# Performance work log

Measured on AMD Instinct MI355X. Metric: run time of the kernel, lower is better.

## Reference

```python
import jax, jax.numpy as jnp
import numpy as np

KH = KW = 5          # deformable kernel (matches offset_channels = 2*5*5)
PAD = 2              # (5-1)//2
DG = 4               # deformable groups


def conv3d(x, w, padding, bias=None):
    # x: [N,C,D,H,W], w: [O,I,kd,kh,kw]
    out = jax.lax.conv_general_dilated(
        x, w, window_strides=(1, 1, 1), padding=padding,
        dimension_numbers=('NCDHW', 'OIDHW', 'NCDHW'))
    if bias is not None:
        out = out + bias[None, :, None, None, None]
    return out


def deform_conv2d(x, offset, weight, pad=PAD, dg=DG):
    """torchvision/mmcv-style deformable conv, stride 1, groups=1, no bias.
    x: [N,C,H,W]; offset: [N, dg*2*K, H, W] ordered (group, k, (dy,dx));
    weight: [Cout, C, KH, KW]."""
    N, C, H, W = x.shape
    K = KH * KW
    off = offset.reshape(N, dg, K, 2, H, W)
    ky, kx = jnp.meshgrid(jnp.arange(KH), jnp.arange(KW), indexing='ij')
    ky = ky.reshape(K).astype(x.dtype)
    kx = kx.reshape(K).astype(x.dtype)
    # absolute sampling positions: [N,dg,K,H,W]
    base_y = ky[:, None, None] - pad + jnp.arange(H, dtype=x.dtype)[None, :, None]
    base_x = kx[:, None, None] - pad + jnp.arange(W, dtype=x.dtype)[None, None, :]
    sy = base_y[None, None] + off[:, :, :, 0]
    sx = base_x[None, None] + off[:, :, :, 1]
    y0 = jnp.floor(sy)
    x0 = jnp.floor(sx)
    wy = sy - y0
    wx = sx - x0
    y0i = y0.astype(jnp.int32)
    x0i = x0.astype(jnp.int32)
    Cg = C // dg
    xg = x.reshape(N, dg, Cg, H * W)

    def gather(yi, xi):
        valid = (yi >= 0) & (yi < H) & (xi >= 0) & (xi < W)
        yc = jnp.clip(yi, 0, H - 1)
        xc = jnp.clip(xi, 0, W - 1)
        idx = (yc * W + xc).reshape(N, dg, 1, K * H * W)
        v = jnp.take_along_axis(xg, idx, axis=3).reshape(N, dg, Cg, K, H, W)
        return v * valid[:, :, None].astype(x.dtype)

    v00 = gather(y0i, x0i)
    v01 = gather(y0i, x0i + 1)
    v10 = gather(y0i + 1, x0i)
    v11 = gather(y0i + 1, x0i + 1)
    wy_ = wy[:, :, None]
    wx_ = wx[:, :, None]
    samp = (v00 * (1 - wy_) * (1 - wx_) + v01 * (1 - wy_) * wx_
            + v10 * wy_ * (1 - wx_) + v11 * wy_ * wx_)
    samp = samp.reshape(N, C, K, H, W)             # deform groups only affect offsets
    wmat = weight.reshape(weight.shape[0], C, K)
    return jnp.einsum('nckhw,ock->nohw', samp, wmat)


def setup_inputs() -> dict:
    key = jax.random.key(0)
    k0, k1, k2, k3, k4 = jax.random.split(key, 5)
    bs, C, T, H, W = 1, 256, 4, 48, 48
    x = jax.random.normal(k0, (bs, C, T, H, W), dtype=jnp.float32)
    # spatio_offset: Conv3d(C -> dg*2*K, kernel (1,5,5), pad (0,2,2), no bias)
    w_off = jax.random.normal(k1, (DG * 2 * KH * KW, C, 1, KH, KW), dtype=jnp.float32) * 0.01
    # spatio_adaption: DeformConv2d weight, init std=0.01 (per init_weights)
    w_def = jax.random.normal(k2, (C, C, KH, KW), dtype=jnp.float32) * 0.01
    # temporal: Conv3d(C -> C, kernel (3,3,3), pad (1,1,1), with bias)
    fan_in = C * 27
    w_temp = jax.random.normal(k3, (C, C, 3, 3, 3), dtype=jnp.float32) * (1.0 / np.sqrt(fan_in))
    b_temp = jax.random.normal(k4, (C,), dtype=jnp.float32) * 0.01
    return {'x': x, 'w_off': w_off, 'w_def': w_def, 'w_temp': w_temp, 'b_temp': b_temp}


def reference(x, w_off, w_def, w_temp, b_temp):
    bs, C, T, H, W = x.shape
    # offset branch uses detached input (torch: x.detach())
    offset = conv3d(jax.lax.stop_gradient(x), w_off, [(0, 0), (PAD, PAD), (PAD, PAD)])
    off_fold = offset.transpose(0, 2, 1, 3, 4).reshape(bs * T, -1, H, W)
    x_fold = x.transpose(0, 2, 1, 3, 4).reshape(bs * T, C, H, W)
    x_spatio_fold = deform_conv2d(x_fold, off_fold, w_def)
    x_spatio = x_spatio_fold.reshape(bs, T, C, H, W).transpose(0, 2, 1, 3, 4)
    # cascaded=False branch: temporal conv on original x, then residual sum
    x_temporal = conv3d(x, w_temp, [(1, 1), (1, 1), (1, 1)], b_temp)
    return x_spatio + x_temporal
```

## Files before the change

### kernel.cpp

```cpp
#include <hip/hip_runtime.h>
#include <hip/hip_bf16.h>

#define T    4
#define C    256
#define H    48
#define W    48
#define HW   2304
#define OFFC 200
#define CK5  6400
#define CK9  2304
#define NFULL 9216
#define BPAD 72

typedef __attribute__((ext_vector_type(8))) short bf16x8;
typedef __attribute__((ext_vector_type(4))) float f32x4;

__device__ __forceinline__ unsigned short f2bf(float f) {
    unsigned int u = __float_as_uint(f);
    return (unsigned short)((u + 0x7FFFu + ((u >> 16) & 1u)) >> 16);
}
__device__ __forceinline__ float bflo(unsigned int v) { return __uint_as_float(v << 16); }
__device__ __forceinline__ float bfhi(unsigned int v) { return __uint_as_float(v & 0xFFFF0000u); }
__device__ __forceinline__ unsigned int pack2(float lo, float hi) {
    __hip_bfloat162 h = __float22bfloat162_rn(make_float2(lo, hi));
    return *reinterpret_cast<unsigned int*>(&h);
}
__device__ __forceinline__ void gload16(const void* g, void* l) {
    __builtin_amdgcn_global_load_lds(
        (const __attribute__((address_space(1))) unsigned int*)g,
        (__attribute__((address_space(3))) unsigned int*)l, 16, 0, 0);
}

__global__ __launch_bounds__(256) void prep_xt_k(const float* __restrict__ x,
                                                 const float* __restrict__ w_off,
                                                 const float* __restrict__ w_def,
                                                 const float* __restrict__ w_temp,
                                                 const float* __restrict__ bias,
                                                 unsigned short* __restrict__ wbo,
                                                 unsigned short* __restrict__ wbd,
                                                 unsigned short* __restrict__ wbT,
                                                 float* __restrict__ offb,
                                                 float* __restrict__ out,
                                                 unsigned short* __restrict__ xt) {
    __shared__ float tile[64][65];
    if (blockIdx.x >= 24320) {
        const int zb = blockIdx.x - 24320;
        const int p0 = (zb % 36) * 64, c0 = ((zb / 36) & 3) * 64, t = zb / 144;
        const int px = threadIdx.x & 63, sub = threadIdx.x >> 6;
        for (int cl = sub; cl < 64; cl += 4)
            tile[px][cl] = x[((long)(c0 + cl) * T + t) * HW + p0 + px];
        __syncthreads();
        const int seg = sub * 16;
        unsigned int pk[8];
        #pragma unroll
        for (int d = 0; d < 8; ++d)
            pk[d] = pack2(tile[px][seg + d * 2], tile[px][seg + d * 2 + 1]);
        unsigned short* orow = xt + ((long)t * HW + p0 + px) * 256 + c0 + seg;
        *(uint4*)(orow + 0) = make_uint4(pk[0], pk[1], pk[2], pk[3]);
        *(uint4*)(orow + 8) = make_uint4(pk[4], pk[5], pk[6], pk[7]);
        return;
    }
    long i = (long)blockIdx.x * 256 + threadIdx.x;
    if (i < 1638400) {
        const int c = (int)(i & 255); const int rest = (int)(i >> 8);
        const int q = rest % 25, o = rest / 25;
        wbo[(long)o * CK5 + q * 256 + c] =
            (o < OFFC) ? f2bf(w_off[((long)o * 256 + c) * 25 + q]) : (unsigned short)0;
    } else if (i < 3276800) {
        i -= 1638400;
        const int c = (int)(i & 255); const int rest = (int)(i >> 8);
        const int q = rest % 25, o = rest / 25;
        wbd[(long)o * CK5 + q * 256 + c] = f2bf(w_def[((long)o * 256 + c) * 25 + q]);
    } else if (i < 5046272) {
        i -= 3276800;
        const int c = (int)(i & 255); const int rest = (int)(i >> 8);
        const int j = rest % 9, oo = rest / 9;
        const int o = oo & 255, kt = oo >> 8;
        wbT[(long)kt * (256 * CK9) + (long)o * CK9 + j * 256 + c] =
            f2bf(w_temp[((long)o * 256 + c) * 27 + kt * 9 + j]);
    } else if (i < 5636096) {
        i -= 5046272;
        ((float4*)offb)[i] = make_float4(0.f, 0.f, 0.f, 0.f);
    } else {
        i -= 5636096;
        const float b = bias[(int)(i / 2304)];
        ((float4*)out)[i] = make_float4(b, b, b, b);
    }
}

__device__ __forceinline__ void mfma_iter_w(const unsigned short* __restrict__ Asl,
                                            const unsigned short* __restrict__ Bsl,
                                            int wave, int quad, int l16, f32x4 acc[4][4]) {
    const int wm = (wave & 1) * 64, wn = (wave >> 1) * 64;
    #pragma unroll
    for (int kh = 0; kh < 2; ++kh) {
        bf16x8 af[4], bfr[4];
        #pragma unroll
        for (int ii = 0; ii < 4; ++ii) {
            const int row = wm + ii * 16 + l16;
            const int slot = (kh * 4 + quad + (l16 & 7)) & 7;
            af[ii] = *(const bf16x8*)(Asl + row * 64 + slot * 8);
        }
        #pragma unroll
        for (int j = 0; j < 4; ++j)
            bfr[j] = *(const bf16x8*)(Bsl + (wn + j * 16 + l16) * BPAD + kh * 32 + quad * 8);
        #pragma unroll
        for (int ii = 0; ii < 4; ++ii)
            #pragma unroll
            for (int j = 0; j < 4; ++j)
                acc[ii][j] = __builtin_amdgcn_mfma_f32_16x16x32_bf16(af[ii], bfr[j], acc[ii][j], 0, 0, 0);
    }
}
__device__ __forceinline__ void epilogue_atomic_w(float* __restrict__ Cf, int m0, int n0,
                                                  int wave, int quad, int l16,
                                                  int Mvalid, f32x4 acc[4][4]) {
    const int wm = (wave & 1) * 64, wn = (wave >> 1) * 64;
    #pragma unroll
    for (int i = 0; i < 4; ++i)
        #pragma unroll
        for (int rr = 0; rr < 4; ++rr) {
            const int o = m0 + wm + i * 16 + quad * 4 + rr;
            if (o >= Mvalid) continue;
            #pragma unroll
            for (int j = 0; j < 4; ++j)
                unsafeAtomicAdd(Cf + (long)o * NFULL + n0 + wn + j * 16 + l16, acc[i][j][rr]);
        }
}

__global__ __launch_bounds__(256, 4) void gemm_off_k(const unsigned short* __restrict__ A,
                                                     const unsigned short* __restrict__ xt,
                                                     float* __restrict__ Cf) {
    __shared__ unsigned short Asl[128 * 64];
    __shared__ unsigned short Bsl[128 * BPAD];
    const int tid = threadIdx.x;
    const int wave = tid >> 6, lane = tid & 63;
    const int quad = lane >> 4, l16 = lane & 15;
    const int n0 = blockIdx.x * 128, m0 = blockIdx.y * 128, k0 = blockIdx.z * 640;
    const int t = n0 / HW, p0 = n0 - t * HW;

    const int r8 = lane >> 3, s8 = lane & 7;
    const int qg = (s8 - r8) & 7;
    const long ldAb = (long)CK5 * 2;
    const char* Ap = (const char*)A + (long)(m0 + wave * 32 + r8) * ldAb
                     + (long)k0 * 2 + qg * 16;
    const long rstep8 = 8 * ldAb;
    unsigned short* la = Asl + wave * 2048;

    const int px = tid >> 1, half = tid & 1;
    const int p = p0 + px, h = p / 48, w = p - h * 48;
    const unsigned short* xts = xt + (long)t * HW * 256 + half * 32;

    auto produce = [&](int kk, uint4 v[4]) {
        const int q = kk >> 8, cb = kk & 255;
        const int d = q / 5;
        const int y = h + d - 2, xx = w + (q - d * 5) - 2;
        v[0] = make_uint4(0u, 0u, 0u, 0u); v[1] = v[0]; v[2] = v[0]; v[3] = v[0];
        if ((y >= 0) & (y < 48) & (xx >= 0) & (xx < 48)) {
            const unsigned short* bp = xts + (y * 48 + xx) * 256 + cb;
            #pragma unroll
            for (int d4 = 0; d4 < 4; ++d4) v[d4] = *(const uint4*)(bp + d4 * 8);
        }
    };

    uint4 cv[4];
    produce(k0, cv);

    f32x4 acc[4][4] = {};
    for (int i = 0; i < 10; ++i) {
        __syncthreads();
        #pragma unroll
        for (int c2 = 0; c2 < 4; ++c2) gload16(Ap + c2 * rstep8, la + c2 * 512);
        Ap += 128;
        #pragma unroll
        for (int d4 = 0; d4 < 4; ++d4)
            *(uint4*)(Bsl + px * BPAD + half * 32 + d4 * 8) = cv[d4];
        __syncthreads();
        if (i + 1 < 10) produce(k0 + (i + 1) * 64, cv);
        mfma_iter_w(Asl, Bsl, wave, quad, l16, acc);
    }
    epilogue_atomic_w(Cf, m0, n0, wave, quad, l16, OFFC, acc);
}

__device__ __forceinline__ void mfma_iter(const unsigned short* __restrict__ Asl,
                                          const unsigned short* __restrict__ Bsl,
                                          int wave, int quad, int l16, f32x4 acc[4][2]) {
    const int wm = (wave & 1) * 64, wn = (wave >> 1) * 32;
    #pragma unroll
    for (int kh = 0; kh < 2; ++kh) {
        bf16x8 af[4], bfr[2];
        #pragma unroll
        for (int i = 0; i < 4; ++i) {
            const int row = wm + i * 16 + l16;
            const int slot = (kh * 4 + quad + (l16 & 7)) & 7;
            af[i] = *(const bf16x8*)(Asl + row * 64 + slot * 8);
        }
        #pragma unroll
        for (int j = 0; j < 2; ++j)
            bfr[j] = *(const bf16x8*)(Bsl + (wn + j * 16 + l16) * BPAD + kh * 32 + quad * 8);
        #pragma unroll
        for (int i = 0; i < 4; ++i)
            #pragma unroll
            for (int j = 0; j < 2; ++j)
                acc[i][j] = __builtin_amdgcn_mfma_f32_16x16x32_bf16(af[i], bfr[j], acc[i][j], 0, 0, 0);
    }
}
__device__ __forceinline__ void epilogue_atomic(float* __restrict__ Cf, int m0, int n0,
                                                int wave, int quad, int l16,
                                                int Mvalid, f32x4 acc[4][2]) {
    const int wm = (wave & 1) * 64, wn = (wave >> 1) * 32;
    #pragma unroll
    for (int i = 0; i < 4; ++i)
        #pragma unroll
        for (int rr = 0; rr < 4; ++rr) {
            const int o = m0 + wm + i * 16 + quad * 4 + rr;
            if (o >= Mvalid) continue;
            #pragma unroll
            for (int j = 0; j < 2; ++j)
                unsafeAtomicAdd(Cf + (long)o * NFULL + n0 + wn + j * 16 + l16, acc[i][j][rr]);
        }
}

__device__ __forceinline__ void pos_calc(int h, int w, int q, float dy, float dx,
                                         float wgt[4], int idx[4]) {
    const int d = q / 5;
    const int qy = d - 2, qx = q - d * 5 - 2;
    const float sy = (float)(h + qy) + dy;
    const float sx = (float)(w + qx) + dx;
    const float y0f = floorf(sy), x0f = floorf(sx);
    const float wy = sy - y0f, wx = sx - x0f;
    const int y0 = (int)y0f, x0 = (int)x0f;
    const int y1 = y0 + 1, x1 = x0 + 1;
    float w00 = (1.f - wy) * (1.f - wx);
    float w01 = (1.f - wy) * wx;
    float w10 = wy * (1.f - wx);
    float w11 = wy * wx;
    const bool vy0 = (y0 >= 0) & (y0 < 48), vy1 = (y1 >= 0) & (y1 < 48);
    const bool vx0 = (x0 >= 0) & (x0 < 48), vx1 = (x1 >= 0) & (x1 < 48);
    if (!(vy0 & vx0)) w00 = 0.f;
    if (!(vy0 & vx1)) w01 = 0.f;
    if (!(vy1 & vx0)) w10 = 0.f;
    if (!(vy1 & vx1)) w11 = 0.f;
    const int yc0 = min(max(y0, 0), 47), yc1 = min(max(y1, 0), 47);
    const int xc0 = min(max(x0, 0), 47), xc1 = min(max(x1, 0), 47);
    wgt[0] = w00; wgt[1] = w01; wgt[2] = w10; wgt[3] = w11;
    idx[0] = yc0 * 48 + xc0; idx[1] = yc0 * 48 + xc1;
    idx[2] = yc1 * 48 + xc0; idx[3] = yc1 * 48 + xc1;
}
__device__ __forceinline__ uint4 blend4(const uint4 u[4], const float wgt[4]) {
    unsigned int pk[4];
    #pragma unroll
    for (int qi = 0; qi < 4; ++qi) {
        const unsigned int a = ((const unsigned int*)&u[0])[qi];
        const unsigned int b = ((const unsigned int*)&u[1])[qi];
        const unsigned int c = ((const unsigned int*)&u[2])[qi];
        const unsigned int d = ((const unsigned int*)&u[3])[qi];
        const float rl = wgt[0] * bflo(a) + wgt[1] * bflo(b) + wgt[2] * bflo(c) + wgt[3] * bflo(d);
        const float rh = wgt[0] * bfhi(a) + wgt[1] * bfhi(b) + wgt[2] * bfhi(c) + wgt[3] * bfhi(d);
        pk[qi] = pack2(rl, rh);
    }
    return make_uint4(pk[0], pk[1], pk[2], pk[3]);
}

__device__ __forceinline__ void gemm_def_body(unsigned short* __restrict__ Asl,
                                              unsigned short* __restrict__ Bsl,
                                              const unsigned short* __restrict__ A,
                                              const unsigned short* __restrict__ xt,
                                              const float* __restrict__ offb,
                                              float* __restrict__ Cf,
                                              int m0, int n0, int k0) {
    const int tid = threadIdx.x;
    const int wave = tid >> 6, lane = tid & 63;
    const int quad = lane >> 4, l16 = lane & 15;
    const int t = n0 / HW, p0 = n0 - t * HW;
    const int px = tid >> 2, seg = tid & 3;
    const int p = p0 + px, h = p / 48, w = p - h * 48;
    const int nabs = n0 + px;
    const unsigned short* xts = xt + (long)t * HW * 256 + seg * 8;

    const int r8 = lane >> 3, s8 = lane & 7;
    const int qg = (s8 - r8) & 7;
    const long ldAb = (long)CK5 * 2;
    const char* Ap = (const char*)A + (long)(m0 + wave * 32 + r8) * ldAb
                     + (long)k0 * 2 + qg * 16;
    const long rstep8 = 8 * ldAb;
    unsigned short* la = Asl + wave * 2048;

    auto off_load = [&](int kk, float& dy, float& dx) {
        const int q = kk >> 8, g = (kk & 255) >> 6;
        dy = offb[(long)(g * 50 + 2 * q) * NFULL + nabs];
        dx = offb[(long)(g * 50 + 2 * q + 1) * NFULL + nabs];
    };
    auto corners = [&](int kk, float dy, float dx, uint4 u[8], float wgt[4]) {
        const int cb = kk & 255;
        int idx[4];
        pos_calc(h, w, kk >> 8, dy, dx, wgt, idx);
        #pragma unroll
        for (int cn = 0; cn < 4; ++cn) {
            const unsigned short* bp = xts + idx[cn] * 256 + cb;
            u[cn]     = *(const uint4*)bp;
            u[cn + 4] = *(const uint4*)(bp + 32);
        }
    };

    uint4 pkv0, pkv1;
    float dyN, dxN;
    {
        float dy0, dx0;
        off_load(k0, dy0, dx0);
        uint4 u[8]; float wg[4];
        corners(k0, dy0, dx0, u, wg);
        pkv0 = blend4(u, wg);
        pkv1 = blend4(u + 4, wg);
        off_load(k0 + 64, dyN, dxN);
    }

    f32x4 acc[4][2] = {};
    for (int i = 0; i < 20; ++i) {
        const int kk = k0 + i * 64;
        __syncthreads();
        #pragma unroll
        for (int c2 = 0; c2 < 4; ++c2) gload16(Ap + c2 * rstep8, la + c2 * 512);
        Ap += 128;
        *(uint4*)(Bsl + px * BPAD + seg * 8)      = pkv0;
        *(uint4*)(Bsl + px * BPAD + 32 + seg * 8) = pkv1;
        __syncthreads();
        const bool more = (i + 1 < 20);
        uint4 u[8]; float wg[4];
        if (more) {
            corners(kk + 64, dyN, dxN, u, wg);
            if (i + 2 < 20) off_load(kk + 128, dyN, dxN);
        }
        mfma_iter(Asl, Bsl, wave, quad, l16, acc);
        if (more) {
            pkv0 = blend4(u, wg);
            pkv1 = blend4(u + 4, wg);
        }
    }
    epilogue_atomic(Cf, m0, n0, wave, quad, l16, C, acc);
}

__device__ __forceinline__ void gemm_temp_body(unsigned short* __restrict__ Asl,
                                               unsigned short* __restrict__ Bsl,
                                               const unsigned short* __restrict__ A,
                                               const unsigned short* __restrict__ xt, int tsrc,
                                               float* __restrict__ Cf,
                                               int m0, int n0, int k0) {
    const int tid = threadIdx.x;
    const int wave = tid >> 6, lane = tid & 63;
    const int quad = lane >> 4, l16 = lane & 15;
    const int t = n0 / HW, p0 = n0 - t * HW;
    const int px = tid >> 1, half = tid & 1;
    const int p = p0 + px, h = p / 48, w = p - h * 48;
    const unsigned short* xts = xt + (long)tsrc * HW * 256 + half * 32;

    const int r8 = lane >> 3, s8 = lane & 7;
    const int qg = (s8 - r8) & 7;
    const long ldAb = (long)CK9 * 2;
    const char* Ap = (const char*)A + (long)(m0 + wave * 32 + r8) * ldAb
                     + (long)k0 * 2 + qg * 16;
    const long rstep8 = 8 * ldAb;
    unsigned short* la = Asl + wave * 2048;

    auto produce = [&](int kk, uint4 v[4]) {
        const int q = kk >> 8, cb = kk & 255;
        const int d = q / 3;
        const int y = h + d - 1, xx = w + (q - d * 3) - 1;
        v[0] = make_uint4(0u, 0u, 0u, 0u); v[1] = v[0]; v[2] = v[0]; v[3] = v[0];
        if ((y >= 0) & (y < 48) & (xx >= 0) & (xx < 48)) {
            const unsigned short* bp = xts + (y * 48 + xx) * 256 + cb;
            #pragma unroll
            for (int d4 = 0; d4 < 4; ++d4) v[d4] = *(const uint4*)(bp + d4 * 8);
        }
    };

    uint4 cv[4];
    produce(k0, cv);

    f32x4 acc[4][4] = {};
    for (int i = 0; i < 18; ++i) {
        __syncthreads();
        #pragma unroll
        for (int c2 = 0; c2 < 4; ++c2) gload16(Ap + c2 * rstep8, la + c2 * 512);
        Ap += 128;
        #pragma unroll
        for (int d4 = 0; d4 < 4; ++d4)
            *(uint4*)(Bsl + px * BPAD + half * 32 + d4 * 8) = cv[d4];
        __syncthreads();
        if (i + 1 < 18) produce(k0 + (i + 1) * 64, cv);
        mfma_iter_w(Asl, Bsl, wave, quad, l16, acc);
    }
    epilogue_atomic_w(Cf, m0, n0, wave, quad, l16, C, acc);
}

__global__ __launch_bounds__(256, 4) void gemm_dt_k(const unsigned short* __restrict__ wbd,
                                                    const unsigned short* __restrict__ wbT,
                                                    const unsigned short* __restrict__ xt,
                                                    const float* __restrict__ offb,
                                                    float* __restrict__ out) {
    __shared__ unsigned short Asl[128 * 64];
    __shared__ unsigned short Bsl[128 * BPAD];
    const int z = blockIdx.z, m0 = blockIdx.y * 128;
    if (z < 5) {
        const int n0 = blockIdx.x * 64;
        gemm_def_body(Asl, Bsl, wbd, xt, offb, out, m0, n0, z * 1280);
    } else {
        if (blockIdx.x >= 72) return;
        const int n0 = blockIdx.x * 128;
        const int zz = z - 5, kt = zz >> 1, half = zz & 1;
        const int t = n0 / HW, tsrc = t + kt - 1;
        if (tsrc < 0 || tsrc >= T) return;
        gemm_temp_body(Asl, Bsl, wbT + (long)kt * 256 * CK9, xt, tsrc, out,
                       m0, n0, half * 1152);
    }
}

extern "C" void kernel_launch(void* const* d_in, const int* in_sizes, int n_in,
                              void* d_out, int out_size, void* d_ws, size_t ws_size,
                              hipStream_t stream) {
    const float* x      = (const float*)d_in[0];
    const float* w_off  = (const float*)d_in[1];
    const float* w_def  = (const float*)d_in[2];
    const float* w_temp = (const float*)d_in[3];
    const float* b_temp = (const float*)d_in[4];
    float* out = (float*)d_out;

    unsigned short* xt   = (unsigned short*)d_ws;
    float*          offb = (float*)((char*)d_ws + 4718592ul);
    unsigned short* wbo  = (unsigned short*)((char*)d_ws + 14155776ul);
    unsigned short* wbd  = (unsigned short*)((char*)d_ws + 17432576ul);
    unsigned short* wbT  = (unsigned short*)((char*)d_ws + 20709376ul);

    prep_xt_k<<<24896, 256, 0, stream>>>(x, w_off, w_def, w_temp, b_temp,
                                         wbo, wbd, wbT, offb, out, xt);
    gemm_off_k<<<dim3(72, 2, 10), 256, 0, stream>>>(wbo, xt, offb);
    gemm_dt_k<<<dim3(144, 2, 11), 256, 0, stream>>>(wbd, wbT, xt, offb, out);
}
```

Baseline: 318.0 us.

## Rebalance temporal-conv GEMM across launches and co-schedule with offset GEMM

The temporal conv taps kt=0 and kt=2 move into the offset-conv GEMM launch, which becomes one fused kernel with 14 z-slices. Only the centre tap kt=1 stays alongside the deformable GEMM, now on 64-wide N tiles with 4x2 accumulators instead of 128-wide. This spreads work more evenly between the two launches and keeps fewer idle or early-exiting blocks in the second grid. The cost is a larger first launch and more atomic traffic from the smaller tiles.

```diff
diff --git a/kernel.cpp b/kernel.cpp
--- a/kernel.cpp
+++ b/kernel.cpp
@@ -127,15 +127,54 @@
         }
 }
 
-__global__ __launch_bounds__(256, 4) void gemm_off_k(const unsigned short* __restrict__ A,
-                                                     const unsigned short* __restrict__ xt,
-                                                     float* __restrict__ Cf) {
-    __shared__ unsigned short Asl[128 * 64];
-    __shared__ unsigned short Bsl[128 * BPAD];
+__device__ __forceinline__ void mfma_iter(const unsigned short* __restrict__ Asl,
+                                          const unsigned short* __restrict__ Bsl,
+                                          int wave, int quad, int l16, f32x4 acc[4][2]) {
+    const int wm = (wave & 1) * 64, wn = (wave >> 1) * 32;
+    #pragma unroll
+    for (int kh = 0; kh < 2; ++kh) {
+        bf16x8 af[4], bfr[2];
+        #pragma unroll
+        for (int i = 0; i < 4; ++i) {
+            const int row = wm + i * 16 + l16;
+            const int slot = (kh * 4 + quad + (l16 & 7)) & 7;
+            af[i] = *(const bf16x8*)(Asl + row * 64 + slot * 8);
+        }
+        #pragma unroll
+        for (int j = 0; j < 2; ++j)
+            bfr[j] = *(const bf16x8*)(Bsl + (wn + j * 16 + l16) * BPAD + kh * 32 + quad * 8);
+        #pragma unroll
+        for (int i = 0; i < 4; ++i)
+            #pragma unroll
+            for (int j = 0; j < 2; ++j)
+                acc[i][j] = __builtin_amdgcn_mfma_f32_16x16x32_bf16(af[i], bfr[j], acc[i][j], 0, 0, 0);
+    }
+}
+__device__ __forceinline__ void epilogue_atomic(float* __restrict__ Cf, int m0, int n0,
+                                                int wave, int quad, int l16,
+                                                int Mvalid, f32x4 acc[4][2]) {
+    const int wm = (wave & 1) * 64, wn = (wave >> 1) * 32;
+    #pragma unroll
+    for (int i = 0; i < 4; ++i)
+        #pragma unroll
+        for (int rr = 0; rr < 4; ++rr) {
+            const int o = m0 + wm + i * 16 + quad * 4 + rr;
+            if (o >= Mvalid) continue;
+            #pragma unroll
+            for (int j = 0; j < 2; ++j)
+                unsafeAtomicAdd(Cf + (long)o * NFULL + n0 + wn + j * 16 + l16, acc[i][j][rr]);
+        }
+}
+
+__device__ __forceinline__ void gemm_off_body(unsigned short* __restrict__ Asl,
+                                              unsigned short* __restrict__ Bsl,
+                                              const unsigned short* __restrict__ A,
+                                              const unsigned short* __restrict__ xt,
+                                              float* __restrict__ Cf,
+                                              int m0, int n0, int k0) {
     const int tid = threadIdx.x;
     const int wave = tid >> 6, lane = tid & 63;
     const int quad = lane >> 4, l16 = lane & 15;
-    const int n0 = blockIdx.x * 128, m0 = blockIdx.y * 128, k0 = blockIdx.z * 640;
     const int t = n0 / HW, p0 = n0 - t * HW;
 
     const int r8 = lane >> 3, s8 = lane & 7;
@@ -181,43 +220,108 @@
     epilogue_atomic_w(Cf, m0, n0, wave, quad, l16, OFFC, acc);
 }
 
-__device__ __forceinline__ void mfma_iter(const unsigned short* __restrict__ Asl,
-                                          const unsigned short* __restrict__ Bsl,
-                                          int wave, int quad, int l16, f32x4 acc[4][2]) {
-    const int wm = (wave & 1) * 64, wn = (wave >> 1) * 32;
-    #pragma unroll
-    for (int kh = 0; kh < 2; ++kh) {
-        bf16x8 af[4], bfr[2];
-        #pragma unroll
-        for (int i = 0; i < 4; ++i) {
-            const int row = wm + i * 16 + l16;
-            const int slot = (kh * 4 + quad + (l16 & 7)) & 7;
-            af[i] = *(const bf16x8*)(Asl + row * 64 + slot * 8);
-        }
-        #pragma unroll
-        for (int j = 0; j < 2; ++j)
-            bfr[j] = *(const bf16x8*)(Bsl + (wn + j * 16 + l16) * BPAD + kh * 32 + quad * 8);
-        #pragma unroll
-        for (int i = 0; i < 4; ++i)
+__device__ __forceinline__ void gemm_temp_body_w(unsigned short* __restrict__ Asl,
+                                                 unsigned short* __restrict__ Bsl,
+                                                 const unsigned short* __restrict__ A,
+                                                 const unsigned short* __restrict__ xt, int tsrc,
+                                                 float* __restrict__ Cf,
+                                                 int m0, int n0, int k0) {
+    const int tid = threadIdx.x;
+    const int wave = tid >> 6, lane = tid & 63;
+    const int quad = lane >> 4, l16 = lane & 15;
+    const int t = n0 / HW, p0 = n0 - t * HW;
+    const int px = tid >> 1, half = tid & 1;
+    const int p = p0 + px, h = p / 48, w = p - h * 48;
+    const unsigned short* xts = xt + (long)tsrc * HW * 256 + half * 32;
+
+    const int r8 = lane >> 3, s8 = lane & 7;
+    const int qg = (s8 - r8) & 7;
+    const long ldAb = (long)CK9 * 2;
+    const char* Ap = (const char*)A + (long)(m0 + wave * 32 + r8) * ldAb
+                     + (long)k0 * 2 + qg * 16;
+    const long rstep8 = 8 * ldAb;
+    unsigned short* la = Asl + wave * 2048;
+
+    auto produce = [&](int kk, uint4 v[4]) {
+        const int q = kk >> 8, cb = kk & 255;
+        const int d = q / 3;
+        const int y = h + d - 1, xx = w + (q - d * 3) - 1;
+        v[0] = make_uint4(0u, 0u, 0u, 0u); v[1] = v[0]; v[2] = v[0]; v[3] = v[0];
+        if ((y >= 0) & (y < 48) & (xx >= 0) & (xx < 48)) {
+            const unsigned short* bp = xts + (y * 48 + xx) * 256 + cb;
             #pragma unroll
-            for (int j = 0; j < 2; ++j)
-                acc[i][j] = __builtin_amdgcn_mfma_f32_16x16x32_bf16(af[i], bfr[j], acc[i][j], 0, 0, 0);
-    }
-}
-__device__ __forceinline__ void epilogue_atomic(float* __restrict__ Cf, int m0, int n0,
-                                                int wave, int quad, int l16,
-                                                int Mvalid, f32x4 acc[4][2]) {
-    const int wm = (wave & 1) * 64, wn = (wave >> 1) * 32;
-    #pragma unroll
-    for (int i = 0; i < 4; ++i)
-        #pragma unroll
-        for (int rr = 0; rr < 4; ++rr) {
-            const int o = m0 + wm + i * 16 + quad * 4 + rr;
-            if (o >= Mvalid) continue;
-            #pragma unroll
-            for (int j = 0; j < 2; ++j)
-                unsafeAtomicAdd(Cf + (long)o * NFULL + n0 + wn + j * 16 + l16, acc[i][j][rr]);
-        }
+            for (int d4 = 0; d4 < 4; ++d4) v[d4] = *(const uint4*)(bp + d4 * 8);
+        }
+    };
+
+    uint4 cv[4];
+    produce(k0, cv);
+
+    f32x4 acc[4][4] = {};
+    for (int i = 0; i < 18; ++i) {
+        __syncthreads();
+        #pragma unroll
+        for (int c2 = 0; c2 < 4; ++c2) gload16(Ap + c2 * rstep8, la + c2 * 512);
+        Ap += 128;
+        #pragma unroll
+        for (int d4 = 0; d4 < 4; ++d4)
+            *(uint4*)(Bsl + px * BPAD + half * 32 + d4 * 8) = cv[d4];
+        __syncthreads();
+        if (i + 1 < 18) produce(k0 + (i + 1) * 64, cv);
+        mfma_iter_w(Asl, Bsl, wave, quad, l16, acc);
+    }
+    epilogue_atomic_w(Cf, m0, n0, wave, quad, l16, C, acc);
+}
+
+__device__ __forceinline__ void gemm_temp_body(unsigned short* __restrict__ Asl,
+                                               unsigned short* __restrict__ Bsl,
+                                               const unsigned short* __restrict__ A,
+                                               const unsigned short* __restrict__ xt, int tsrc,
+                                               float* __restrict__ Cf,
+                                               int m0, int n0, int k0) {
+    const int tid = threadIdx.x;
+    const int wave = tid >> 6, lane = tid & 63;
+    const int quad = lane >> 4, l16 = lane & 15;
+    const int t = n0 / HW, p0 = n0 - t * HW;
+    const int px = tid >> 2, seg = tid & 3;
+    const int p = p0 + px, h = p / 48, w = p - h * 48;
+    const unsigned short* xts = xt + (long)tsrc * HW * 256 + seg * 8;
+
+    const int r8 = lane >> 3, s8 = lane & 7;
+    const int qg = (s8 - r8) & 7;
+    const long ldAb = (long)CK9 * 2;
+    const char* Ap = (const char*)A + (long)(m0 + wave * 32 + r8) * ldAb
+                     + (long)k0 * 2 + qg * 16;
+    const long rstep8 = 8 * ldAb;
+    unsigned short* la = Asl + wave * 2048;
+
+    auto produce = [&](int kk, uint4& v0, uint4& v1) {
+        const int q = kk >> 8, cb = kk & 255;
+        const int d = q / 3;
+        const int y = h + d - 1, xx = w + (q - d * 3) - 1;
+        v0 = make_uint4(0u, 0u, 0u, 0u); v1 = v0;
+        if ((y >= 0) & (y < 48) & (xx >= 0) & (xx < 48)) {
+            const unsigned short* bp = xts + (y * 48 + xx) * 256 + cb;
+            v0 = *(const uint4*)bp; v1 = *(const uint4*)(bp + 32);
+        }
+    };
+
+    uint4 cv0, cv1;
+    produce(k0, cv0, cv1);
+
+    f32x4 acc[4][2] = {};
+    for (int i = 0; i < 18; ++i) {
+        __syncthreads();
+        #pragma unroll
+        for (int c2 = 0; c2 < 4; ++c2) gload16(Ap + c2 * rstep8, la + c2 * 512);
+        Ap += 128;
+        *(uint4*)(Bsl + px * BPAD + seg * 8)      = cv0;
+        *(uint4*)(Bsl + px * BPAD + 32 + seg * 8) = cv1;
+        __syncthreads();
+        if (i + 1 < 18) produce(k0 + (i + 1) * 64, cv0, cv1);
+        mfma_iter(Asl, Bsl, wave, quad, l16, acc);
+    }
+    epilogue_atomic(Cf, m0, n0, wave, quad, l16, C, acc);
 }
 
 __device__ __forceinline__ void pos_calc(int h, int w, int q, float dy, float dx,
@@ -339,57 +443,24 @@
     epilogue_atomic(Cf, m0, n0, wave, quad, l16, C, acc);
 }
 
-__device__ __forceinline__ void gemm_temp_body(unsigned short* __restrict__ Asl,
-                                               unsigned short* __restrict__ Bsl,
-                                               const unsigned short* __restrict__ A,
-                                               const unsigned short* __restrict__ xt, int tsrc,
-                                               float* __restrict__ Cf,
-                                               int m0, int n0, int k0) {
-    const int tid = threadIdx.x;
-    const int wave = tid >> 6, lane = tid & 63;
-    const int quad = lane >> 4, l16 = lane & 15;
-    const int t = n0 / HW, p0 = n0 - t * HW;
-    const int px = tid >> 1, half = tid & 1;
-    const int p = p0 + px, h = p / 48, w = p - h * 48;
-    const unsigned short* xts = xt + (long)tsrc * HW * 256 + half * 32;
-
-    const int r8 = lane >> 3, s8 = lane & 7;
-    const int qg = (s8 - r8) & 7;
-    const long ldAb = (long)CK9 * 2;
-    const char* Ap = (const char*)A + (long)(m0 + wave * 32 + r8) * ldAb
-                     + (long)k0 * 2 + qg * 16;
-    const long rstep8 = 8 * ldAb;
-    unsigned short* la = Asl + wave * 2048;
-
-    auto produce = [&](int kk, uint4 v[4]) {
-        const int q = kk >> 8, cb = kk & 255;
-        const int d = q / 3;
-        const int y = h + d - 1, xx = w + (q - d * 3) - 1;
-        v[0] = make_uint4(0u, 0u, 0u, 0u); v[1] = v[0]; v[2] = v[0]; v[3] = v[0];
-        if ((y >= 0) & (y < 48) & (xx >= 0) & (xx < 48)) {
-            const unsigned short* bp = xts + (y * 48 + xx) * 256 + cb;
-            #pragma unroll
-            for (int d4 = 0; d4 < 4; ++d4) v[d4] = *(const uint4*)(bp + d4 * 8);
-        }
-    };
-
-    uint4 cv[4];
-    produce(k0, cv);
-
-    f32x4 acc[4][4] = {};
-    for (int i = 0; i < 18; ++i) {
-        __syncthreads();
-        #pragma unroll
-        for (int c2 = 0; c2 < 4; ++c2) gload16(Ap + c2 * rstep8, la + c2 * 512);
-        Ap += 128;
-        #pragma unroll
-        for (int d4 = 0; d4 < 4; ++d4)
-            *(uint4*)(Bsl + px * BPAD + half * 32 + d4 * 8) = cv[d4];
-        __syncthreads();
-        if (i + 1 < 18) produce(k0 + (i + 1) * 64, cv);
-        mfma_iter_w(Asl, Bsl, wave, quad, l16, acc);
-    }
-    epilogue_atomic_w(Cf, m0, n0, wave, quad, l16, C, acc);
+__global__ __launch_bounds__(256, 4) void gemm_offt_k(const unsigned short* __restrict__ wbo,
+                                                      const unsigned short* __restrict__ wbT,
+                                                      const unsigned short* __restrict__ xt,
+                                                      float* __restrict__ offb,
+                                                      float* __restrict__ out) {
+    __shared__ unsigned short Asl[128 * 64];
+    __shared__ unsigned short Bsl[128 * BPAD];
+    const int z = blockIdx.z, n0 = blockIdx.x * 128, m0 = blockIdx.y * 128;
+    if (z < 10) {
+        gemm_off_body(Asl, Bsl, wbo, xt, offb, m0, n0, z * 640);
+    } else {
+        const int zz = z - 10;
+        const int kt = (zz < 2) ? 0 : 2, half = zz & 1;
+        const int t = n0 / HW, tsrc = t + kt - 1;
+        if (tsrc < 0 || tsrc >= T) return;
+        gemm_temp_body_w(Asl, Bsl, wbT + (long)kt * 256 * CK9, xt, tsrc, out,
+                         m0, n0, half * 1152);
+    }
 }
 
 __global__ __launch_bounds__(256, 4) void gemm_dt_k(const unsigned short* __restrict__ wbd,
@@ -398,18 +469,14 @@
                                                     const float* __restrict__ offb,
                                                     float* __restrict__ out) {
     __shared__ unsigned short Asl[128 * 64];
-    __shared__ unsigned short Bsl[128 * BPAD];
-    const int z = blockIdx.z, m0 = blockIdx.y * 128;
+    __shared__ unsigned short Bsl[64 * BPAD];
+    const int z = blockIdx.z, n0 = blockIdx.x * 64, m0 = blockIdx.y * 128;
     if (z < 5) {
-        const int n0 = blockIdx.x * 64;
         gemm_def_body(Asl, Bsl, wbd, xt, offb, out, m0, n0, z * 1280);
     } else {
-        if (blockIdx.x >= 72) return;
-        const int n0 = blockIdx.x * 128;
-        const int zz = z - 5, kt = zz >> 1, half = zz & 1;
-        const int t = n0 / HW, tsrc = t + kt - 1;
-        if (tsrc < 0 || tsrc >= T) return;
-        gemm_temp_body(Asl, Bsl, wbT + (long)kt * 256 * CK9, xt, tsrc, out,
+        const int half = z - 5;
+        const int t = n0 / HW;
+        gemm_temp_body(Asl, Bsl, wbT + (long)1 * 256 * CK9, xt, t, out,
                        m0, n0, half * 1152);
     }
 }
@@ -432,6 +499,6 @@
 
     prep_xt_k<<<24896, 256, 0, stream>>>(x, w_off, w_def, w_temp, b_temp,
                                          wbo, wbd, wbT, offb, out, xt);
-    gemm_off_k<<<dim3(72, 2, 10), 256, 0, stream>>>(wbo, xt, offb);
-    gemm_dt_k<<<dim3(144, 2, 11), 256, 0, stream>>>(wbd, wbT, xt, offb, out);
-}
+    gemm_offt_k<<<dim3(72, 2, 14), 256, 0, stream>>>(wbo, wbT, xt, offb, out);
+    gemm_dt_k<<<dim3(144, 2, 7), 256, 0, stream>>>(wbd, wbT, xt, offb, out);
+}
```

Result: no change. 317.9 us (-0.0%).
